# Kernel optimization log

Measured on AMD Instinct MI355X. Metric: run time of the kernel, lower is better.

Reference implementation:

```python
import jax, jax.numpy as jnp
import numpy as np

B, T, C = 4, 2048, 1024
N_HEAD = 16


def setup_inputs() -> dict:
    key = jax.random.key(0)
    k1, k2, k3, k4, k5 = jax.random.split(key, 5)
    x = jax.random.normal(k1, (B, T, C), dtype=jnp.float32)
    # c_attn: Dense(3*C) -> kernel [C, 3C], bias [3C]
    w_attn = jax.random.normal(k2, (C, 3 * C), dtype=jnp.float32) * 0.02
    b_attn = jnp.zeros((3 * C,), dtype=jnp.float32)
    # c_proj: Dense(C) with scaled init 0.02/sqrt(2*n_layer), n_layer=24
    w_proj = jax.random.normal(k3, (C, C), dtype=jnp.float32) * (0.02 / np.sqrt(2 * 24))
    b_proj = jnp.zeros((C,), dtype=jnp.float32)
    return {"x": x, "w_attn": w_attn, "b_attn": b_attn, "w_proj": w_proj, "b_proj": b_proj}


def reference(x, w_attn, b_attn, w_proj, b_proj):
    Bx, Tx, Cx = x.shape
    hd = Cx // N_HEAD  # head dim
    qkv = x @ w_attn + b_attn                      # [B, T, 3C]
    q, k, v = jnp.split(qkv, 3, axis=2)
    q = q.reshape(Bx, Tx, N_HEAD, hd).transpose(0, 2, 1, 3)  # [B, H, T, hd]
    k = k.reshape(Bx, Tx, N_HEAD, hd).transpose(0, 2, 1, 3)
    v = v.reshape(Bx, Tx, N_HEAD, hd).transpose(0, 2, 1, 3)
    mask = jnp.tril(jnp.ones((1, 1, Tx, Tx), dtype=bool))
    att = jnp.einsum('bhqd,bhkd->bhqk', q, k) / jnp.sqrt(jnp.float32(hd))
    att = jnp.where(mask, att, jnp.finfo(jnp.float32).min)
    att = jax.nn.softmax(att, axis=-1)
    y = jnp.einsum('bhqk,bhkd->bhqd', att, v)      # [B, H, T, hd]
    y = y.transpose(0, 2, 1, 3).reshape(Bx, Tx, Cx)
    return y @ w_proj + b_proj
```

## Files before the change

### kernel.cpp

```cpp
#include <hip/hip_runtime.h>
#include <cstdint>
#include <cstddef>

typedef unsigned short u16;
typedef __bf16 bf16_t;
typedef bf16_t bf16x8 __attribute__((ext_vector_type(8)));
typedef float f32x4 __attribute__((ext_vector_type(4)));
typedef float f32x16 __attribute__((ext_vector_type(16)));

__device__ __forceinline__ u16 f32_to_bf16(float f) {
  uint32_t u = __builtin_bit_cast(uint32_t, f);
  u += 0x7fffu + ((u >> 16) & 1u);
  return (u16)(u >> 16);
}

__device__ __forceinline__ uint32_t pack_bf16x2(float lo, float hi) {
  uint32_t a = __builtin_bit_cast(uint32_t, hi) + 0x8000u;
  uint32_t b = __builtin_bit_cast(uint32_t, lo) + 0x8000u;
  return __builtin_amdgcn_perm(a, b, 0x07060302u);
}

__device__ __forceinline__ void gload_lds16(const void* g, void* l) {
  __builtin_amdgcn_global_load_lds(
      (const __attribute__((address_space(1))) unsigned int*)g,
      (__attribute__((address_space(3))) unsigned int*)l, 16, 0, 0);
}

__global__ void cvt_bf16(const float* __restrict__ in, u16* __restrict__ out, int n) {
  int i = (blockIdx.x * 256 + threadIdx.x) * 4;
  if (i < n) {
    float4 f = *(const float4*)(in + i);
    ushort4 o;
    o.x = f32_to_bf16(f.x); o.y = f32_to_bf16(f.y);
    o.z = f32_to_bf16(f.z); o.w = f32_to_bf16(f.w);
    *(ushort4*)(out + i) = o;
  }
}

__global__ void tconv(const float* __restrict__ in, u16* __restrict__ out, int R, int C) {
  __shared__ u16 t[64][80];
  int tid = threadIdx.x;
  int cb = blockIdx.x * 64, rb = blockIdx.y * 64;
  int rr = tid >> 2, cg = (tid & 3) * 16;
  const float* ip = in + (size_t)(rb + rr) * C + cb + cg;
#pragma unroll
  for (int i = 0; i < 16; ++i) t[rr][cg + i] = f32_to_bf16(ip[i]);
  __syncthreads();
  int cc = tid >> 2, rg = (tid & 3) * 16;
  u16* op = out + (size_t)(cb + cc) * R + rb + rg;
  union { uint4 v[2]; u16 s[16]; } tmp;
#pragma unroll
  for (int i = 0; i < 16; ++i) tmp.s[i] = t[rg + i][cc];
  *(uint4*)op = tmp.v[0];
  *(uint4*)(op + 8) = tmp.v[1];
}

__global__ void vtrans(const u16* __restrict__ qkvb, u16* __restrict__ vt) {
  __shared__ u16 t[64][80];
  int tid = threadIdx.x;
  int bh = blockIdx.x, tb = blockIdx.y * 64;
  int b = bh >> 4, h = bh & 15;
  int tt = tid >> 2, dg = (tid & 3) * 16;
  const u16* ip = qkvb + (size_t)(b * 2048 + tb + tt) * 3072 + 2048 + h * 64 + dg;
  union { uint4 v; u16 s[8]; } a0, a1;
  a0.v = *(const uint4*)ip;
  a1.v = *(const uint4*)(ip + 8);
#pragma unroll
  for (int i = 0; i < 8; ++i) { t[tt][dg + i] = a0.s[i]; t[tt][dg + 8 + i] = a1.s[i]; }
  __syncthreads();
  int dd = tid >> 2, tg = (tid & 3) * 16;
  u16* op = vt + (size_t)(bh * 64 + dd) * 2048 + tb + tg;
  union { uint4 v[2]; u16 s[16]; } tmp;
#pragma unroll
  for (int i = 0; i < 16; ++i) {
    int pi = (i & 3) | ((i & 4) << 1) | ((i & 8) >> 1);
    tmp.s[i] = t[tg + pi][dd];
  }
  *(uint4*)op = tmp.v[0];
  *(uint4*)(op + 8) = tmp.v[1];
}

template <int OUT_BF16>
__global__ __launch_bounds__(512, 2) void gemm256(const u16* __restrict__ A,
                                                  const u16* __restrict__ Bt,
                                                  const float* __restrict__ bias,
                                                  void* __restrict__ Cout,
                                                  int M, int N, int K) {
  __shared__ __align__(16) u16 lds[2][2][16384];
  const int tid = threadIdx.x;
  const int w = tid >> 6, L = tid & 63;
  const int quad = L >> 4, lc = L & 15;
  const int wr = w >> 2, wc = w & 3;
  const int wrM = wr * 128, wcN = wc * 64;
  const int rL = L >> 3;
  const int gsw = (L & 7) ^ rL;

  const int nbx = N >> 8;
  const int cpx = gridDim.x >> 3;
  const int id = blockIdx.x;
  const int swz = (id & 7) * cpx + (id >> 3);
  const int tileN = (swz % nbx) << 8;
  const int tileM = (swz / nbx) << 8;
  const int nkt = K >> 6;

  u16* const A0 = &lds[0][0][0];
  u16* const B0 = &lds[0][1][0];
  u16* const A1 = &lds[1][0][0];
  u16* const B1 = &lds[1][1][0];

  auto stageQ = [&](const u16* Mp, int gRow, int kt, u16* reg) {
    int ktc = kt < nkt ? kt : nkt - 1;
    const u16* src = Mp + (size_t)(gRow + w * 8 + rL) * K + (ktc << 6) + gsw * 8;
    gload_lds16(src, reg + w * 512);
  };

  f32x4 acc[8][4] = {};
  const int rsw = lc & 7;
  const int g0 = (quad ^ rsw) * 8;
  const int g1 = ((4 + quad) ^ rsw) * 8;
  const int aRow = (wrM + lc) * 64;
  const int bRow = (wcN + lc) * 64;

  stageQ(A, tileM + 0, 0, A0 + 0);
  stageQ(A, tileM + 128, 0, A0 + 8192);
  stageQ(Bt, tileN + 0, 0, B0 + 0);
  stageQ(Bt, tileN + 64, 0, B0 + 4096);
  stageQ(A, tileM + 64, 0, A0 + 4096);
  stageQ(A, tileM + 192, 0, A0 + 12288);
  stageQ(Bt, tileN + 128, 0, B0 + 8192);
  stageQ(Bt, tileN + 192, 0, B0 + 12288);
  stageQ(A, tileM + 0, 1, A1 + 0);
  stageQ(A, tileM + 128, 1, A1 + 8192);
  stageQ(Bt, tileN + 0, 1, B1 + 0);
  stageQ(Bt, tileN + 64, 1, B1 + 4096);
  stageQ(A, tileM + 64, 1, A1 + 4096);
  stageQ(A, tileM + 192, 1, A1 + 12288);
  asm volatile("s_waitcnt vmcnt(6)" ::: "memory");
  __builtin_amdgcn_s_barrier();

  auto group = [&](u16* Ab, u16* Bb, u16* Bob, int T) {
    bf16x8 af[4][2], blo[2][2], bhi[2][2];
#pragma unroll
    for (int mi = 0; mi < 4; ++mi) {
      af[mi][0] = *(const bf16x8*)&Ab[aRow + mi * 1024 + g0];
      af[mi][1] = *(const bf16x8*)&Ab[aRow + mi * 1024 + g1];
    }
#pragma unroll
    for (int ni = 0; ni < 2; ++ni) {
      blo[ni][0] = *(const bf16x8*)&Bb[bRow + ni * 1024 + g0];
      blo[ni][1] = *(const bf16x8*)&Bb[bRow + ni * 1024 + g1];
    }
    stageQ(Bt, tileN + 128, T + 1, Bob + 8192);
    stageQ(Bt, tileN + 192, T + 1, Bob + 12288);
    asm volatile("" ::: "memory");
    __builtin_amdgcn_s_barrier();
    asm volatile("s_waitcnt lgkmcnt(0)" ::: "memory");
    __builtin_amdgcn_s_setprio(1);
#pragma unroll
    for (int mi = 0; mi < 4; ++mi)
#pragma unroll
      for (int ni = 0; ni < 2; ++ni) {
        acc[mi][ni] = __builtin_amdgcn_mfma_f32_16x16x32_bf16(af[mi][0], blo[ni][0], acc[mi][ni], 0, 0, 0);
        acc[mi][ni] = __builtin_amdgcn_mfma_f32_16x16x32_bf16(af[mi][1], blo[ni][1], acc[mi][ni], 0, 0, 0);
      }
    __builtin_amdgcn_s_setprio(0);
    asm volatile("" ::: "memory");
    __builtin_amdgcn_s_barrier();
#pragma unroll
    for (int ni = 0; ni < 2; ++ni) {
      bhi[ni][0] = *(const bf16x8*)&Bb[bRow + (2 + ni) * 1024 + g0];
      bhi[ni][1] = *(const bf16x8*)&Bb[bRow + (2 + ni) * 1024 + g1];
    }
    stageQ(A, tileM + 0, T + 2, Ab + 0);
    stageQ(A, tileM + 128, T + 2, Ab + 8192);
    asm volatile("" ::: "memory");
    __builtin_amdgcn_s_barrier();
    asm volatile("s_waitcnt lgkmcnt(0)" ::: "memory");
    __builtin_amdgcn_s_setprio(1);
#pragma unroll
    for (int mi = 0; mi < 4; ++mi)
#pragma unroll
      for (int ni = 0; ni < 2; ++ni) {
        acc[mi][ni + 2] = __builtin_amdgcn_mfma_f32_16x16x32_bf16(af[mi][0], bhi[ni][0], acc[mi][ni + 2], 0, 0, 0);
        acc[mi][ni + 2] = __builtin_amdgcn_mfma_f32_16x16x32_bf16(af[mi][1], bhi[ni][1], acc[mi][ni + 2], 0, 0, 0);
      }
    __builtin_amdgcn_s_setprio(0);
    asm volatile("" ::: "memory");
    __builtin_amdgcn_s_barrier();
#pragma unroll
    for (int mi = 0; mi < 4; ++mi) {
      af[mi][0] = *(const bf16x8*)&Ab[aRow + (4 + mi) * 1024 + g0];
      af[mi][1] = *(const bf16x8*)&Ab[aRow + (4 + mi) * 1024 + g1];
    }
    stageQ(Bt, tileN + 0, T + 2, Bb + 0);
    stageQ(Bt, tileN + 64, T + 2, Bb + 4096);
    asm volatile("" ::: "memory");
    __builtin_amdgcn_s_barrier();
    asm volatile("s_waitcnt lgkmcnt(0)" ::: "memory");
    __builtin_amdgcn_s_setprio(1);
#pragma unroll
    for (int mi = 0; mi < 4; ++mi)
#pragma unroll
      for (int ni = 0; ni < 2; ++ni) {
        acc[mi + 4][ni + 2] = __builtin_amdgcn_mfma_f32_16x16x32_bf16(af[mi][0], bhi[ni][0], acc[mi + 4][ni + 2], 0, 0, 0);
        acc[mi + 4][ni + 2] = __builtin_amdgcn_mfma_f32_16x16x32_bf16(af[mi][1], bhi[ni][1], acc[mi + 4][ni + 2], 0, 0, 0);
      }
    __builtin_amdgcn_s_setprio(0);
    asm volatile("" ::: "memory");
    __builtin_amdgcn_s_barrier();
    stageQ(A, tileM + 64, T + 2, Ab + 4096);
    stageQ(A, tileM + 192, T + 2, Ab + 12288);
    asm volatile("" ::: "memory");
    __builtin_amdgcn_s_barrier();
    __builtin_amdgcn_s_setprio(1);
#pragma unroll
    for (int mi = 0; mi < 4; ++mi)
#pragma unroll
      for (int ni = 0; ni < 2; ++ni) {
        acc[mi + 4][ni] = __builtin_amdgcn_mfma_f32_16x16x32_bf16(af[mi][0], blo[ni][0], acc[mi + 4][ni], 0, 0, 0);
        acc[mi + 4][ni] = __builtin_amdgcn_mfma_f32_16x16x32_bf16(af[mi][1], blo[ni][1], acc[mi + 4][ni], 0, 0, 0);
      }
    __builtin_amdgcn_s_setprio(0);
    asm volatile("s_waitcnt vmcnt(6)" ::: "memory");
    __builtin_amdgcn_s_barrier();
  };

  for (int T = 0; T < nkt; T += 2) {
    group(A0, B0, B1, T);
    group(A1, B1, B0, T + 1);
  }

  asm volatile("s_waitcnt vmcnt(0)" ::: "memory");

#pragma unroll
  for (int mi = 0; mi < 8; ++mi) {
    int rowb = tileM + wrM + mi * 16 + quad * 4;
#pragma unroll
    for (int ni = 0; ni < 4; ++ni) {
      int col = tileN + wcN + ni * 16 + lc;
      float bv = bias[col];
#pragma unroll
      for (int r = 0; r < 4; ++r) {
        float v = acc[mi][ni][r] + bv;
        if (OUT_BF16)
          ((u16*)Cout)[(size_t)(rowb + r) * N + col] = f32_to_bf16(v);
        else
          ((float*)Cout)[(size_t)(rowb + r) * N + col] = v;
      }
    }
  }
}

__global__ __launch_bounds__(512, 4) void attn(const u16* __restrict__ qkvb,
                                               const u16* __restrict__ vt,
                                               u16* __restrict__ yb) {
  __shared__ __align__(16) u16 kv[2][16][512];
  const int tid = threadIdx.x;
  const int w = tid >> 6, L = tid & 63;
  const int l5 = L & 31, hi = L >> 5;
  const int bh = blockIdx.x;
  const int b = bh >> 4, h = bh & 15;
  const int qt = (blockIdx.y < 4) ? (7 - blockIdx.y) : (blockIdx.y - 4);
  const float e_c = 0.18033688f;
  const int qbase = qt * 256;
  const int wq = qbase + w * 32;
  const int nk = qbase + 256;

  const int u = w - 4;
  const u16* kb0 = qkvb + (size_t)(b * 2048 + (w >> 1) * 32 + l5) * 3072 + 1024 +
                   h * 64 + (w & 1) * 32 + hi * 8;
  const u16* vb0 = vt + (size_t)(bh * 64 + (u >> 1) * 32 + l5) * 2048 +
                   (u & 1) * 32 + hi * 8;

  auto stage = [&](int kb2, int buf) {
    if (w < 4) {
      const u16* s = kb0 + (size_t)kb2 * 3072;
      gload_lds16(s, &kv[buf][2 * w][0]);
      gload_lds16(s + 16, &kv[buf][2 * w + 1][0]);
    } else {
      const u16* s = vb0 + kb2;
      gload_lds16(s, &kv[buf][8 + 2 * u][0]);
      gload_lds16(s + 16, &kv[buf][8 + 2 * u + 1][0]);
    }
  };

  const int qrow = wq + l5;
  bf16x8 qf[4];
  {
    const u16* qp = qkvb + ((size_t)(b * 2048 + qrow) * 3072 + h * 64 + hi * 8);
#pragma unroll
    for (int ds = 0; ds < 4; ++ds) qf[ds] = *(const bf16x8*)(qp + ds * 16);
  }
  f32x16 o0 = {}, o1 = {};
  float lsum = 0.f;

  int par = 0;
  stage(0, 0);

  for (int kb = 0; kb < nk; kb += 64) {
    __syncthreads();
    stage((kb + 64 < nk) ? kb + 64 : 0, par ^ 1);

    if (kb <= wq + 31) {
      const bool part = (kb + 63 > wq);
      const int lim = qrow - 4 * hi - kb;

      f32x16 st0 = {}, st1 = {};
      __builtin_amdgcn_s_setprio(1);
#pragma unroll
      for (int ds = 0; ds < 4; ++ds) {
        bf16x8 k0 = *(const bf16x8*)&kv[par][ds][L * 8];
        bf16x8 k1 = *(const bf16x8*)&kv[par][4 + ds][L * 8];
        st0 = __builtin_amdgcn_mfma_f32_32x32x16_bf16(k0, qf[ds], st0, 0, 0, 0);
        st1 = __builtin_amdgcn_mfma_f32_32x32x16_bf16(k1, qf[ds], st1, 0, 0, 0);
      }
      __builtin_amdgcn_s_setprio(0);

#pragma unroll
      for (int r = 0; r < 16; ++r) {
        float p0 = __builtin_amdgcn_exp2f(st0[r] * e_c);
        float p1 = __builtin_amdgcn_exp2f(st1[r] * e_c);
        if (part) {
          const int br = (r & 3) + 8 * (r >> 2);
          p0 = (br <= lim) ? p0 : 0.f;
          p1 = (32 + br <= lim) ? p1 : 0.f;
        }
        st0[r] = p0;
        st1[r] = p1;
        lsum += p0 + p1;
      }

      __builtin_amdgcn_s_setprio(1);
#pragma unroll
      for (int sg = 0; sg < 2; ++sg) {
        union { uint32_t u[4]; bf16x8 v; } pf0, pf1;
#pragma unroll
        for (int q2 = 0; q2 < 4; ++q2) {
          pf0.u[q2] = pack_bf16x2(st0[sg * 8 + q2 * 2], st0[sg * 8 + q2 * 2 + 1]);
          pf1.u[q2] = pack_bf16x2(st1[sg * 8 + q2 * 2], st1[sg * 8 + q2 * 2 + 1]);
        }
        const int ks0 = sg, ks1 = 2 + sg;
        bf16x8 va = *(const bf16x8*)&kv[par][8 + ks0][L * 8];
        bf16x8 vb = *(const bf16x8*)&kv[par][12 + ks0][L * 8];
        o0 = __builtin_amdgcn_mfma_f32_32x32x16_bf16(va, pf0.v, o0, 0, 0, 0);
        o1 = __builtin_amdgcn_mfma_f32_32x32x16_bf16(vb, pf0.v, o1, 0, 0, 0);
        va = *(const bf16x8*)&kv[par][8 + ks1][L * 8];
        vb = *(const bf16x8*)&kv[par][12 + ks1][L * 8];
        o0 = __builtin_amdgcn_mfma_f32_32x32x16_bf16(va, pf1.v, o0, 0, 0, 0);
        o1 = __builtin_amdgcn_mfma_f32_32x32x16_bf16(vb, pf1.v, o1, 0, 0, 0);
      }
      __builtin_amdgcn_s_setprio(0);
    }

    par ^= 1;
  }

  lsum += __shfl_xor(lsum, 32);
  float inv = 1.f / lsum;

  u16* yp = yb + (size_t)(b * 2048 + qrow) * 1024 + h * 64 + hi * 4;
#pragma unroll
  for (int g = 0; g < 4; ++g) {
    uint2 pk;
    pk.x = pack_bf16x2(o0[g * 4 + 0] * inv, o0[g * 4 + 1] * inv);
    pk.y = pack_bf16x2(o0[g * 4 + 2] * inv, o0[g * 4 + 3] * inv);
    *(uint2*)(yp + g * 8) = pk;
    pk.x = pack_bf16x2(o1[g * 4 + 0] * inv, o1[g * 4 + 1] * inv);
    pk.y = pack_bf16x2(o1[g * 4 + 2] * inv, o1[g * 4 + 3] * inv);
    *(uint2*)(yp + 32 + g * 8) = pk;
  }

  asm volatile("s_waitcnt vmcnt(0)" ::: "memory");
}

extern "C" void kernel_launch(void* const* d_in, const int* in_sizes, int n_in,
                              void* d_out, int out_size, void* d_ws, size_t ws_size,
                              hipStream_t stream) {
  const float* x = (const float*)d_in[0];
  const float* w_attn = (const float*)d_in[1];
  const float* b_attn = (const float*)d_in[2];
  const float* w_proj = (const float*)d_in[3];
  const float* b_proj = (const float*)d_in[4];
  float* out = (float*)d_out;

  char* ws = (char*)d_ws;
  u16* xb = (u16*)ws;    ws += (size_t)8192 * 1024 * 2;
  u16* waT = (u16*)ws;   ws += (size_t)3072 * 1024 * 2;
  u16* wpT = (u16*)ws;   ws += (size_t)1024 * 1024 * 2;
  u16* qkvb = (u16*)ws;  ws += (size_t)8192 * 3072 * 2;
  u16* vtb = (u16*)ws;   ws += (size_t)64 * 64 * 2048 * 2;
  u16* yb = (u16*)ws;    ws += (size_t)8192 * 1024 * 2;

  cvt_bf16<<<8192, 256, 0, stream>>>(x, xb, 8192 * 1024);
  tconv<<<dim3(3072 / 64, 1024 / 64), 256, 0, stream>>>(w_attn, waT, 1024, 3072);
  tconv<<<dim3(1024 / 64, 1024 / 64), 256, 0, stream>>>(w_proj, wpT, 1024, 1024);
  gemm256<1><<<dim3(384), 512, 0, stream>>>(xb, waT, b_attn, qkvb, 8192, 3072, 1024);
  vtrans<<<dim3(64, 32), 256, 0, stream>>>(qkvb, vtb);
  attn<<<dim3(64, 8), 512, 0, stream>>>(qkvb, vtb, yb);
  gemm256<0><<<dim3(128), 512, 0, stream>>>(yb, wpT, b_proj, out, 8192, 1024, 1024);
}
```

Baseline: 258.0 us.

## Use 128x256-tile GEMM for output projection to fill more CUs

Adds a gemm128 kernel with 128x256 output tiles, a double-buffered LDS pipeline and interleaved stage/MFMA phases. The output projection now uses it with 256 blocks instead of 128 blocks of the 256-tile kernel. The aim is better occupancy across the 256 CUs of the MI355X for this small GEMM. The cost is less data reuse per tile and more global loads of the B operand.

```diff
diff --git a/kernel.cpp b/kernel.cpp
--- a/kernel.cpp
+++ b/kernel.cpp
@@ -251,6 +251,171 @@
   }
 }
 
+template <int OUT_BF16>
+__global__ __launch_bounds__(512, 2) void gemm128(const u16* __restrict__ A,
+                                                  const u16* __restrict__ Bt,
+                                                  const float* __restrict__ bias,
+                                                  void* __restrict__ Cout,
+                                                  int M, int N, int K) {
+  __shared__ __align__(16) u16 Abuf[2][8192];
+  __shared__ __align__(16) u16 Bbuf[2][16384];
+  const int tid = threadIdx.x;
+  const int w = tid >> 6, L = tid & 63;
+  const int quad = L >> 4, lc = L & 15;
+  const int wr = w >> 2, wc = w & 3;
+  const int rL = L >> 3;
+  const int gsw = (L & 7) ^ rL;
+
+  const int nbx = N >> 8;
+  const int cpx = gridDim.x >> 3;
+  const int id = blockIdx.x;
+  const int swz = (id & 7) * cpx + (id >> 3);
+  const int tileN = (swz % nbx) << 8;
+  const int tileM = (swz / nbx) << 7;
+  const int nkt = K >> 6;
+
+  u16* const A0 = &Abuf[0][0];
+  u16* const A1 = &Abuf[1][0];
+  u16* const B0 = &Bbuf[0][0];
+  u16* const B1 = &Bbuf[1][0];
+
+  auto stageQ = [&](const u16* Mp, int gRow, int kt, u16* dst) {
+    int ktc = kt < nkt ? kt : nkt - 1;
+    const u16* src = Mp + (size_t)(gRow + w * 8 + rL) * K + (ktc << 6) + gsw * 8;
+    gload_lds16(src, dst + w * 512);
+  };
+
+  f32x4 acc[4][4] = {};
+  const int rsw = lc & 7;
+  const int g0 = (quad ^ rsw) * 8;
+  const int g1 = ((4 + quad) ^ rsw) * 8;
+  const int aRow = (wr * 64 + lc) * 64;
+  const int bRow = (wc * 64 + lc) * 64;
+
+  stageQ(A, tileM + 0, 0, A0 + 0);
+  stageQ(A, tileM + 64, 0, A0 + 4096);
+  stageQ(Bt, tileN + 0, 0, B0 + 0);
+  stageQ(Bt, tileN + 64, 0, B0 + 4096);
+  stageQ(Bt, tileN + 128, 0, B0 + 8192);
+  stageQ(Bt, tileN + 192, 0, B0 + 12288);
+  stageQ(Bt, tileN + 0, 1, B1 + 0);
+  stageQ(Bt, tileN + 64, 1, B1 + 4096);
+  stageQ(A, tileM + 0, 1, A1 + 0);
+  stageQ(A, tileM + 64, 1, A1 + 4096);
+  asm volatile("s_waitcnt vmcnt(4)" ::: "memory");
+  __builtin_amdgcn_s_barrier();
+
+  auto group = [&](u16* Ab, u16* Bb, u16* OBb, int T) {
+    bf16x8 alo[2][2], ahi[2][2], blo[2][2], bhi[2][2];
+#pragma unroll
+    for (int mi = 0; mi < 2; ++mi) {
+      alo[mi][0] = *(const bf16x8*)&Ab[aRow + mi * 1024 + g0];
+      alo[mi][1] = *(const bf16x8*)&Ab[aRow + mi * 1024 + g1];
+    }
+#pragma unroll
+    for (int ni = 0; ni < 2; ++ni) {
+      blo[ni][0] = *(const bf16x8*)&Bb[bRow + ni * 1024 + g0];
+      blo[ni][1] = *(const bf16x8*)&Bb[bRow + ni * 1024 + g1];
+    }
+    stageQ(Bt, tileN + 128, T + 1, OBb + 8192);
+    stageQ(Bt, tileN + 192, T + 1, OBb + 12288);
+    asm volatile("" ::: "memory");
+    __builtin_amdgcn_s_barrier();
+    asm volatile("s_waitcnt lgkmcnt(0)" ::: "memory");
+    __builtin_amdgcn_s_setprio(1);
+#pragma unroll
+    for (int mi = 0; mi < 2; ++mi)
+#pragma unroll
+      for (int ni = 0; ni < 2; ++ni) {
+        acc[mi][ni] = __builtin_amdgcn_mfma_f32_16x16x32_bf16(alo[mi][0], blo[ni][0], acc[mi][ni], 0, 0, 0);
+        acc[mi][ni] = __builtin_amdgcn_mfma_f32_16x16x32_bf16(alo[mi][1], blo[ni][1], acc[mi][ni], 0, 0, 0);
+      }
+    __builtin_amdgcn_s_setprio(0);
+    asm volatile("" ::: "memory");
+    __builtin_amdgcn_s_barrier();
+#pragma unroll
+    for (int ni = 0; ni < 2; ++ni) {
+      bhi[ni][0] = *(const bf16x8*)&Bb[bRow + (2 + ni) * 1024 + g0];
+      bhi[ni][1] = *(const bf16x8*)&Bb[bRow + (2 + ni) * 1024 + g1];
+    }
+    asm volatile("" ::: "memory");
+    __builtin_amdgcn_s_barrier();
+    asm volatile("s_waitcnt lgkmcnt(0)" ::: "memory");
+    __builtin_amdgcn_s_setprio(1);
+#pragma unroll
+    for (int mi = 0; mi < 2; ++mi)
+#pragma unroll
+      for (int ni = 0; ni < 2; ++ni) {
+        acc[mi][ni + 2] = __builtin_amdgcn_mfma_f32_16x16x32_bf16(alo[mi][0], bhi[ni][0], acc[mi][ni + 2], 0, 0, 0);
+        acc[mi][ni + 2] = __builtin_amdgcn_mfma_f32_16x16x32_bf16(alo[mi][1], bhi[ni][1], acc[mi][ni + 2], 0, 0, 0);
+      }
+    __builtin_amdgcn_s_setprio(0);
+    asm volatile("" ::: "memory");
+    __builtin_amdgcn_s_barrier();
+#pragma unroll
+    for (int mi = 0; mi < 2; ++mi) {
+      ahi[mi][0] = *(const bf16x8*)&Ab[aRow + (2 + mi) * 1024 + g0];
+      ahi[mi][1] = *(const bf16x8*)&Ab[aRow + (2 + mi) * 1024 + g1];
+    }
+    stageQ(Bt, tileN + 0, T + 2, Bb + 0);
+    stageQ(Bt, tileN + 64, T + 2, Bb + 4096);
+    asm volatile("" ::: "memory");
+    __builtin_amdgcn_s_barrier();
+    asm volatile("s_waitcnt lgkmcnt(0)" ::: "memory");
+    __builtin_amdgcn_s_setprio(1);
+#pragma unroll
+    for (int mi = 0; mi < 2; ++mi)
+#pragma unroll
+      for (int ni = 0; ni < 2; ++ni) {
+        acc[mi + 2][ni + 2] = __builtin_amdgcn_mfma_f32_16x16x32_bf16(ahi[mi][0], bhi[ni][0], acc[mi + 2][ni + 2], 0, 0, 0);
+        acc[mi + 2][ni + 2] = __builtin_amdgcn_mfma_f32_16x16x32_bf16(ahi[mi][1], bhi[ni][1], acc[mi + 2][ni + 2], 0, 0, 0);
+      }
+    __builtin_amdgcn_s_setprio(0);
+    asm volatile("" ::: "memory");
+    __builtin_amdgcn_s_barrier();
+    stageQ(A, tileM + 0, T + 2, Ab + 0);
+    stageQ(A, tileM + 64, T + 2, Ab + 4096);
+    asm volatile("" ::: "memory");
+    __builtin_amdgcn_s_barrier();
+    __builtin_amdgcn_s_setprio(1);
+#pragma unroll
+    for (int mi = 0; mi < 2; ++mi)
+#pragma unroll
+      for (int ni = 0; ni < 2; ++ni) {
+        acc[mi + 2][ni] = __builtin_amdgcn_mfma_f32_16x16x32_bf16(ahi[mi][0], blo[ni][0], acc[mi + 2][ni], 0, 0, 0);
+        acc[mi + 2][ni] = __builtin_amdgcn_mfma_f32_16x16x32_bf16(ahi[mi][1], blo[ni][1], acc[mi + 2][ni], 0, 0, 0);
+      }
+    __builtin_amdgcn_s_setprio(0);
+    asm volatile("s_waitcnt vmcnt(4)" ::: "memory");
+    __builtin_amdgcn_s_barrier();
+  };
+
+  for (int T = 0; T < nkt; T += 2) {
+    group(A0, B0, B1, T);
+    group(A1, B1, B0, T + 1);
+  }
+
+  asm volatile("s_waitcnt vmcnt(0)" ::: "memory");
+
+#pragma unroll
+  for (int mi = 0; mi < 4; ++mi) {
+    int rowb = tileM + wr * 64 + mi * 16 + quad * 4;
+#pragma unroll
+    for (int ni = 0; ni < 4; ++ni) {
+      int col = tileN + wc * 64 + ni * 16 + lc;
+      float bv = bias[col];
+#pragma unroll
+      for (int r = 0; r < 4; ++r) {
+        float v = acc[mi][ni][r] + bv;
+        if (OUT_BF16)
+          ((u16*)Cout)[(size_t)(rowb + r) * N + col] = f32_to_bf16(v);
+        else
+          ((float*)Cout)[(size_t)(rowb + r) * N + col] = v;
+      }
+    }
+  }
+}
+
 __global__ __launch_bounds__(512, 4) void attn(const u16* __restrict__ qkvb,
                                                const u16* __restrict__ vt,
                                                u16* __restrict__ yb) {
@@ -397,5 +562,5 @@
   gemm256<1><<<dim3(384), 512, 0, stream>>>(xb, waT, b_attn, qkvb, 8192, 3072, 1024);
   vtrans<<<dim3(64, 32), 256, 0, stream>>>(qkvb, vtb);
   attn<<<dim3(64, 8), 512, 0, stream>>>(qkvb, vtb, yb);
-  gemm256<0><<<dim3(128), 512, 0, stream>>>(yb, wpT, b_proj, out, 8192, 1024, 1024);
-}
+  gemm128<0><<<dim3(256), 512, 0, stream>>>(yb, wpT, b_proj, out, 8192, 1024, 1024);
+}
```

Measured after the change: 246.5 us. 4.5% less time.
